# Performance work log

Measured on AMD Instinct MI355X. Metric: run time of the kernel, lower is better.

Reference implementation:

```python
import jax, jax.numpy as jnp
import numpy as np

D = 1024      # n_embedding
H = 16        # n_head
DH = D // H   # head_size = 64
T = 2048      # block_size / seq len
B = 2
EPS = 1e-5


def layer_norm(x, gamma, beta):
    mu = jnp.mean(x, axis=-1, keepdims=True)
    var = jnp.mean((x - mu) ** 2, axis=-1, keepdims=True)
    return (x - mu) * jax.lax.rsqrt(var + EPS) * gamma + beta


def setup_inputs() -> dict:
    key = jax.random.key(0)
    ks = jax.random.split(key, 12)
    s = 0.02
    return {
        "x": jax.random.normal(ks[0], (B, T, D), jnp.float32),
        # per-head QKV projections stacked over heads: [H, D, DH] (no bias, as in Head)
        "wq": jax.random.normal(ks[1], (H, D, DH), jnp.float32) * s,
        "wk": jax.random.normal(ks[2], (H, D, DH), jnp.float32) * s,
        "wv": jax.random.normal(ks[3], (H, D, DH), jnp.float32) * s,
        # output projection [H*DH, D] with bias
        "w_proj": jax.random.normal(ks[4], (H * DH, D), jnp.float32) * s,
        "b_proj": jnp.zeros((D,), jnp.float32),
        # feedforward: D -> 4D -> D
        "w1": jax.random.normal(ks[5], (D, 4 * D), jnp.float32) * s,
        "b1": jnp.zeros((4 * D,), jnp.float32),
        "w2": jax.random.normal(ks[6], (4 * D, D), jnp.float32) * s,
        "b2": jnp.zeros((D,), jnp.float32),
        # layer norms
        "ln1_g": jnp.ones((D,), jnp.float32),
        "ln1_b": jnp.zeros((D,), jnp.float32),
        "ln2_g": jnp.ones((D,), jnp.float32),
        "ln2_b": jnp.zeros((D,), jnp.float32),
    }


def reference(x, wq, wk, wv, w_proj, b_proj, w1, b1, w2, b2,
              ln1_g, ln1_b, ln2_g, ln2_b):
    # pre-LN attention sub-block
    xn = layer_norm(x, ln1_g, ln1_b)                      # [B,T,D]
    q = jnp.einsum('btd,hdk->bhtk', xn, wq)               # [B,H,T,DH]
    k = jnp.einsum('btd,hdk->bhtk', xn, wk)
    v = jnp.einsum('btd,hdk->bhtk', xn, wv)
    scale = DH ** -0.5
    scores = jnp.einsum('bhtk,bhsk->bhts', q, k) * scale  # [B,H,T,T]
    causal = jnp.tril(jnp.ones((T, T), bool))
    scores = jnp.where(causal, scores, -jnp.inf)
    attn = jax.nn.softmax(scores, axis=-1)
    out = jnp.einsum('bhts,bhsk->bhtk', attn, v)          # [B,H,T,DH]
    out = out.transpose(0, 2, 1, 3).reshape(B, T, H * DH)  # concat heads
    x = x + out @ w_proj + b_proj                          # residual 1
    # pre-LN feedforward sub-block
    xn2 = layer_norm(x, ln2_g, ln2_b)
    h = jax.nn.relu(xn2 @ w1 + b1)
    x = x + h @ w2 + b2                                    # residual 2
    return x
```

## Files before the change

### kernel.cpp

```cpp
#include <hip/hip_runtime.h>
#include <hip/hip_bf16.h>
#include <math.h>


#define D_MODEL 1024
#define NH 16
#define DHEAD 64
#define SEQ 2048
#define NTOK 4096

typedef __bf16 bf16x8 __attribute__((ext_vector_type(8)));
typedef float f32x4 __attribute__((ext_vector_type(4)));
typedef unsigned short u16x8 __attribute__((ext_vector_type(8)));

__device__ __forceinline__ unsigned short f2b(float f) {
  unsigned u = __builtin_bit_cast(unsigned, f);
  u = u + 0x7fffu + ((u >> 16) & 1u);
  return (unsigned short)(u >> 16);
}

__device__ __forceinline__ bf16x8 ld_bf16x8(const unsigned short* p) {
  u16x8 u = *(const u16x8*)p;
  return __builtin_bit_cast(bf16x8, u);
}

__device__ __forceinline__ void async16(void* lds, const void* g) {
  __builtin_amdgcn_global_load_lds(
      (const __attribute__((address_space(1))) unsigned int*)g,
      (__attribute__((address_space(3))) unsigned int*)lds, 16, 0, 0);
}


__global__ __launch_bounds__(256) void repack_qkv(
    const float* __restrict__ wq, const float* __restrict__ wk,
    const float* __restrict__ wv, unsigned short* __restrict__ outT) {
  __shared__ float tile[64][65];
  int t = blockIdx.x;
  int sel = t >> 8;
  int h = (t >> 4) & 15;
  int rt = t & 15;
  const float* in = (sel == 0 ? wq : sel == 1 ? wk : wv) + (size_t)h * D_MODEL * DHEAD;
  int d0 = rt * 64;
  for (int i = 0; i < 16; i++) {
    int idx = i * 256 + threadIdx.x;
    int r = idx >> 6, c = idx & 63;
    tile[r][c] = in[(size_t)(d0 + r) * DHEAD + c];
  }
  __syncthreads();
  unsigned short* ob = outT + (size_t)(sel * 1024 + h * 64) * D_MODEL + d0;
  for (int i = 0; i < 16; i++) {
    int idx = i * 256 + threadIdx.x;
    int c = idx >> 6, r = idx & 63;
    ob[(size_t)c * D_MODEL + r] = f2b(tile[r][c]);
  }
}

__global__ __launch_bounds__(256) void transpose_to_bf16(
    const float* __restrict__ in, unsigned short* __restrict__ out, int R, int C) {
  __shared__ float tile[64][65];
  int r0 = blockIdx.x * 64, c0 = blockIdx.y * 64;
  for (int i = 0; i < 16; i++) {
    int idx = i * 256 + threadIdx.x;
    int r = idx >> 6, c = idx & 63;
    tile[r][c] = in[(size_t)(r0 + r) * C + c0 + c];
  }
  __syncthreads();
  for (int i = 0; i < 16; i++) {
    int idx = i * 256 + threadIdx.x;
    int c = idx >> 6, r = idx & 63;
    out[(size_t)(c0 + c) * R + r0 + r] = f2b(tile[r][c]);
  }
}

__global__ __launch_bounds__(256) void layernorm_bf16(
    const float* __restrict__ x, const float* __restrict__ g,
    const float* __restrict__ bta, unsigned short* __restrict__ out) {
  int row = blockIdx.x;
  int tid = threadIdx.x;
  const float4* xr = (const float4*)(x + (size_t)row * D_MODEL);
  float4 v = xr[tid];
  float s = v.x + v.y + v.z + v.w;
  float s2 = v.x * v.x + v.y * v.y + v.z * v.z + v.w * v.w;
  for (int m = 1; m < 64; m <<= 1) {
    s += __shfl_xor(s, m);
    s2 += __shfl_xor(s2, m);
  }
  __shared__ float ps[4], ps2[4];
  int wid = tid >> 6;
  if ((tid & 63) == 0) { ps[wid] = s; ps2[wid] = s2; }
  __syncthreads();
  float S = ps[0] + ps[1] + ps[2] + ps[3];
  float S2 = ps2[0] + ps2[1] + ps2[2] + ps2[3];
  float mu = S * (1.f / D_MODEL);
  float var = S2 * (1.f / D_MODEL) - mu * mu;
  float inv = rsqrtf(var + 1e-5f);
  float4 gv = ((const float4*)g)[tid];
  float4 bv = ((const float4*)bta)[tid];
  ushort4 o;
  o.x = f2b((v.x - mu) * inv * gv.x + bv.x);
  o.y = f2b((v.y - mu) * inv * gv.y + bv.y);
  o.z = f2b((v.z - mu) * inv * gv.z + bv.z);
  o.w = f2b((v.w - mu) * inv * gv.w + bv.w);
  ((ushort4*)(out + (size_t)row * D_MODEL))[tid] = o;
}

template <int MODE>
__global__ __launch_bounds__(256, 2) void gemm_bt(
    const unsigned short* __restrict__ A, const unsigned short* __restrict__ BT,
    int M, int N, int K,
    const float* __restrict__ bias, const float* __restrict__ resid,
    float* __restrict__ outF, unsigned short* __restrict__ outB,
    unsigned short* __restrict__ outQ, unsigned short* __restrict__ outK,
    unsigned short* __restrict__ outV) {
  __shared__ alignas(16) unsigned short lsA[128 * 64];
  __shared__ alignas(16) unsigned short lsB[128 * 64];
  const int tid = threadIdx.x;
  const int wid = tid >> 6, lane = tid & 63;
  const int lr = lane & 15, lg = lane >> 4;
  const int row0 = blockIdx.x * 128, col0 = blockIdx.y * 128;
  const int wr = (wid >> 1) * 64, wc = (wid & 1) * 64;
  f32x4 acc[4][4] = {};
  const int nk = K >> 6;
  for (int kt = 0; kt < nk; ++kt) {
    const int k0 = kt << 6;
    if (kt) __syncthreads();
#pragma unroll
    for (int i = 0; i < 4; i++) {
      int sidx = i * 256 + tid;
      int r = sidx >> 3, s = sidx & 7;
      int ss = s ^ (r & 7);
      async16((char*)lsA + (i * 256 + wid * 64) * 16,
              A + (size_t)(row0 + r) * K + k0 + ss * 8);
      async16((char*)lsB + (i * 256 + wid * 64) * 16,
              BT + (size_t)(col0 + r) * K + k0 + ss * 8);
    }
    __syncthreads();
#pragma unroll
    for (int kk = 0; kk < 2; ++kk) {
      bf16x8 af[4], bfr[4];
#pragma unroll
      for (int m = 0; m < 4; m++) {
        int r = wr + m * 16 + lr;
        int sw = (kk * 4 + lg) ^ (r & 7);
        af[m] = *(const bf16x8*)((const char*)lsA + r * 128 + sw * 16);
      }
#pragma unroll
      for (int n = 0; n < 4; n++) {
        int r = wc + n * 16 + lr;
        int sw = (kk * 4 + lg) ^ (r & 7);
        bfr[n] = *(const bf16x8*)((const char*)lsB + r * 128 + sw * 16);
      }
#pragma unroll
      for (int m = 0; m < 4; m++)
#pragma unroll
        for (int n = 0; n < 4; n++)
          acc[m][n] = __builtin_amdgcn_mfma_f32_16x16x32_bf16(af[m], bfr[n], acc[m][n], 0, 0, 0);
    }
  }
#pragma unroll
  for (int m = 0; m < 4; m++) {
#pragma unroll
    for (int n = 0; n < 4; n++) {
#pragma unroll
      for (int r2 = 0; r2 < 4; r2++) {
        int row = row0 + wr + m * 16 + lg * 4 + r2;
        int col = col0 + wc + n * 16 + lr;
        float v = acc[m][n][r2];
        if constexpr (MODE == 0) {
          v += bias[col] + resid[(size_t)row * N + col];
          outF[(size_t)row * N + col] = v;
        } else if constexpr (MODE == 1) {
          v += bias[col];
          v = fmaxf(v, 0.f);
          outB[(size_t)row * N + col] = f2b(v);
        } else {
          int sel = col >> 10, jj = col & 1023, h = jj >> 6, dh = jj & 63;
          int b = row >> 11, t = row & 2047;
          size_t bh = (size_t)(b * NH + h);
          if (sel == 0)      outQ[(bh * SEQ + t) * DHEAD + dh] = f2b(v);
          else if (sel == 1) outK[(bh * SEQ + t) * DHEAD + dh] = f2b(v);
          else               outV[(bh * DHEAD + dh) * SEQ + t] = f2b(v);
        }
      }
    }
  }
}

__global__ __launch_bounds__(512, 2) void gemm_bt8(
    const unsigned short* __restrict__ A, const unsigned short* __restrict__ BT,
    int M, int N, int K,
    const float* __restrict__ bias, const float* __restrict__ resid,
    float* __restrict__ outF) {
  __shared__ alignas(16) unsigned short lsA[128 * 64];
  __shared__ alignas(16) unsigned short lsB[128 * 64];
  const int tid = threadIdx.x;
  const int wid = tid >> 6, lane = tid & 63;
  const int lr = lane & 15, lg = lane >> 4;
  const int row0 = blockIdx.x * 128, col0 = blockIdx.y * 128;
  const int wr = (wid >> 2) * 64, wc = (wid & 3) * 32;
  f32x4 acc[4][2] = {};
  const int nk = K >> 6;
  for (int kt = 0; kt < nk; ++kt) {
    const int k0 = kt << 6;
    if (kt) __syncthreads();
#pragma unroll
    for (int i = 0; i < 2; i++) {
      int sidx = i * 512 + tid;
      int r = sidx >> 3, s = sidx & 7;
      int ss = s ^ (r & 7);
      async16((char*)lsA + (i * 512 + wid * 64) * 16,
              A + (size_t)(row0 + r) * K + k0 + ss * 8);
      async16((char*)lsB + (i * 512 + wid * 64) * 16,
              BT + (size_t)(col0 + r) * K + k0 + ss * 8);
    }
    __syncthreads();
#pragma unroll
    for (int kk = 0; kk < 2; ++kk) {
      bf16x8 af[4], bfr[2];
#pragma unroll
      for (int m = 0; m < 4; m++) {
        int r = wr + m * 16 + lr;
        int sw = (kk * 4 + lg) ^ (r & 7);
        af[m] = *(const bf16x8*)((const char*)lsA + r * 128 + sw * 16);
      }
#pragma unroll
      for (int n = 0; n < 2; n++) {
        int r = wc + n * 16 + lr;
        int sw = (kk * 4 + lg) ^ (r & 7);
        bfr[n] = *(const bf16x8*)((const char*)lsB + r * 128 + sw * 16);
      }
#pragma unroll
      for (int m = 0; m < 4; m++)
#pragma unroll
        for (int n = 0; n < 2; n++)
          acc[m][n] = __builtin_amdgcn_mfma_f32_16x16x32_bf16(af[m], bfr[n], acc[m][n], 0, 0, 0);
    }
  }
#pragma unroll
  for (int m = 0; m < 4; m++) {
#pragma unroll
    for (int n = 0; n < 2; n++) {
#pragma unroll
      for (int r2 = 0; r2 < 4; r2++) {
        int row = row0 + wr + m * 16 + lg * 4 + r2;
        int col = col0 + wc + n * 16 + lr;
        float v = acc[m][n][r2] + bias[col] + resid[(size_t)row * N + col];
        outF[(size_t)row * N + col] = v;
      }
    }
  }
}

__global__ __launch_bounds__(512, 2) void gemm256_bt(
    const unsigned short* __restrict__ A, const unsigned short* __restrict__ BT,
    int M, int N, int K, int ntn,
    const float* __restrict__ bias, unsigned short* __restrict__ outB) {
  __shared__ alignas(16) unsigned short ls[2][2][2][256 * 32];
  const int tid = threadIdx.x;
  const int wid = tid >> 6, lane = tid & 63;
  const int lr = lane & 15, lg = lane >> 4;
  const int nwg = gridDim.x;
  const int wg = (blockIdx.x & 7) * (nwg >> 3) + (blockIdx.x >> 3);
  const int row0 = (wg / ntn) * 256, col0 = (wg % ntn) * 256;
  const int mbase = (wid >> 2) * 128;
  const int nbase = (wid & 3) * 64;

  f32x4 acc[8][4] = {};

  auto STAGE = [&](int buf, int kh, int ab, int kt) {
    const unsigned short* src = ab ? (BT + (size_t)col0 * K) : (A + (size_t)row0 * K);
    const int kbase = kt * 64 + kh * 32;
    unsigned short* dst0 = &ls[buf][kh][ab][0];
#pragma unroll
    for (int c = 0; c < 2; c++) {
      int s = c * 512 + tid;
      int row = s >> 2, c2 = s & 3;
      int ss = c2 ^ ((row >> 1) & 3);
      async16(dst0 + (size_t)(c * 512 + wid * 64) * 8,
              src + (size_t)row * K + kbase + ss * 8);
    }
  };
  auto LDA = [&](bf16x8* a, int buf, int kk, int mh) {
#pragma unroll
    for (int i = 0; i < 4; i++) {
      int mrow = mbase + (mh * 4 + i) * 16 + lr;
      int ch = lg ^ ((mrow >> 1) & 3);
      a[i] = *(const bf16x8*)&ls[buf][kk][0][mrow * 32 + ch * 8];
    }
  };
  auto LDB = [&](bf16x8* b, int buf, int kk) {
#pragma unroll
    for (int i = 0; i < 4; i++) {
      int brow = nbase + i * 16 + lr;
      int ch = lg ^ ((brow >> 1) & 3);
      b[i] = *(const bf16x8*)&ls[buf][kk][1][brow * 32 + ch * 8];
    }
  };

  const int nk = K >> 6;
  STAGE(0, 0, 0, 0); STAGE(0, 0, 1, 0); STAGE(0, 1, 0, 0); STAGE(0, 1, 1, 0);
  asm volatile("s_waitcnt vmcnt(4)" ::: "memory");
  __builtin_amdgcn_s_barrier();

  for (int t = 0; t < nk; ++t) {
    const int cur = t & 1, nxt = cur ^ 1;
    const bool haveNext = (t + 1 < nk);
    bf16x8 a[4], b[4];
    LDA(a, cur, 0, 0); LDB(b, cur, 0);
    if (haveNext) STAGE(nxt, 0, 0, t + 1);
    __builtin_amdgcn_s_barrier();
    asm volatile("s_waitcnt lgkmcnt(0)" ::: "memory");
    __builtin_amdgcn_sched_barrier(0);
    __builtin_amdgcn_s_setprio(1);
#pragma unroll
    for (int i = 0; i < 4; i++)
#pragma unroll
      for (int j = 0; j < 4; j++)
        acc[i][j] = __builtin_amdgcn_mfma_f32_16x16x32_bf16(a[i], b[j], acc[i][j], 0, 0, 0);
    __builtin_amdgcn_s_setprio(0);
    __builtin_amdgcn_s_barrier();
    LDA(a, cur, 0, 1);
    if (haveNext) {
      STAGE(nxt, 0, 1, t + 1);
      asm volatile("s_waitcnt vmcnt(4)" ::: "memory");
    } else {
      asm volatile("s_waitcnt vmcnt(0)" ::: "memory");
    }
    __builtin_amdgcn_s_barrier();
    asm volatile("s_waitcnt lgkmcnt(0)" ::: "memory");
    __builtin_amdgcn_sched_barrier(0);
    __builtin_amdgcn_s_setprio(1);
#pragma unroll
    for (int i = 0; i < 4; i++)
#pragma unroll
      for (int j = 0; j < 4; j++)
        acc[4 + i][j] = __builtin_amdgcn_mfma_f32_16x16x32_bf16(a[i], b[j], acc[4 + i][j], 0, 0, 0);
    __builtin_amdgcn_s_setprio(0);
    __builtin_amdgcn_s_barrier();
    LDA(a, cur, 1, 0); LDB(b, cur, 1);
    if (haveNext) STAGE(nxt, 1, 0, t + 1);
    __builtin_amdgcn_s_barrier();
    asm volatile("s_waitcnt lgkmcnt(0)" ::: "memory");
    __builtin_amdgcn_sched_barrier(0);
    __builtin_amdgcn_s_setprio(1);
#pragma unroll
    for (int i = 0; i < 4; i++)
#pragma unroll
      for (int j = 0; j < 4; j++)
        acc[i][j] = __builtin_amdgcn_mfma_f32_16x16x32_bf16(a[i], b[j], acc[i][j], 0, 0, 0);
    __builtin_amdgcn_s_setprio(0);
    __builtin_amdgcn_s_barrier();
    LDA(a, cur, 1, 1);
    if (haveNext) {
      STAGE(nxt, 1, 1, t + 1);
      asm volatile("s_waitcnt vmcnt(4)" ::: "memory");
    }
    __builtin_amdgcn_s_barrier();
    asm volatile("s_waitcnt lgkmcnt(0)" ::: "memory");
    __builtin_amdgcn_sched_barrier(0);
    __builtin_amdgcn_s_setprio(1);
#pragma unroll
    for (int i = 0; i < 4; i++)
#pragma unroll
      for (int j = 0; j < 4; j++)
        acc[4 + i][j] = __builtin_amdgcn_mfma_f32_16x16x32_bf16(a[i], b[j], acc[4 + i][j], 0, 0, 0);
    __builtin_amdgcn_s_setprio(0);
    __builtin_amdgcn_s_barrier();
  }
#pragma unroll
  for (int mi = 0; mi < 8; mi++) {
#pragma unroll
    for (int ni = 0; ni < 4; ni++) {
#pragma unroll
      for (int r2 = 0; r2 < 4; r2++) {
        int row = row0 + mbase + mi * 16 + lg * 4 + r2;
        int col = col0 + nbase + ni * 16 + lr;
        float v = acc[mi][ni][r2] + bias[col];
        outB[(size_t)row * N + col] = f2b(fmaxf(v, 0.f));
      }
    }
  }
}

__global__ __launch_bounds__(256) void attn_fwd(
    const unsigned short* __restrict__ Q, const unsigned short* __restrict__ K,
    const unsigned short* __restrict__ VT, unsigned short* __restrict__ O) {
  __shared__ alignas(16) unsigned short Kl[2][4096];
  __shared__ alignas(16) unsigned short Vl[2][4096];
  __shared__ alignas(16) unsigned short Plds[4][16][72];
  const int tid = threadIdx.x, wid = tid >> 6, lane = tid & 63;
  const int lr = lane & 15, lg = lane >> 4;
  const int sid = (int)(blockIdx.x & 7) * 128 + (int)(blockIdx.x >> 3);
  const int bh = sid >> 5, qt = 31 - (sid & 31);
  const unsigned short* Qb = Q + (size_t)bh * SEQ * DHEAD;
  const unsigned short* Kb = K + (size_t)bh * SEQ * DHEAD;
  const unsigned short* Vb = VT + (size_t)bh * DHEAD * SEQ;
  const int q0 = qt * 64 + wid * 16;
  bf16x8 qf[2];
#pragma unroll
  for (int kk = 0; kk < 2; kk++)
    qf[kk] = ld_bf16x8(Qb + (size_t)(q0 + lr) * DHEAD + kk * 32 + lg * 8);
  float psum[4] = {0.f, 0.f, 0.f, 0.f};
  f32x4 o[4] = {};
  const float cs = 0.18033688011112042f;
  const int ntiles = qt + 1;

  auto STAGE = [&](unsigned short* Kd, unsigned short* Vd, int s0) {
#pragma unroll
    for (int c = 0; c < 2; c++) {
      int s = c * 256 + tid;
      int row = s >> 3, sl = s & 7;
      int ss = sl ^ (row & 7);
      async16((char*)Kd + (c * 256 + wid * 64) * 16,
              Kb + (size_t)(s0 + row) * DHEAD + ss * 8);
      async16((char*)Vd + (c * 256 + wid * 64) * 16,
              Vb + (size_t)row * SEQ + s0 + ss * 8);
    }
  };

  STAGE(Kl[0], Vl[0], 0);
  for (int t = 0; t < ntiles; ++t) {
    if (t + 1 < ntiles) {
      STAGE(Kl[(t + 1) & 1], Vl[(t + 1) & 1], (t + 1) * 64);
      asm volatile("s_waitcnt vmcnt(4)" ::: "memory");
    } else {
      asm volatile("s_waitcnt vmcnt(0)" ::: "memory");
    }
    __builtin_amdgcn_s_barrier();
    __builtin_amdgcn_sched_barrier(0);
    const unsigned short* Kc = Kl[t & 1];
    const unsigned short* Vc = Vl[t & 1];
    const int s0 = t * 64;
    f32x4 sf[4];
#pragma unroll
    for (int n = 0; n < 4; n++) {
      f32x4 a = {};
#pragma unroll
      for (int kk = 0; kk < 2; kk++) {
        int r = n * 16 + lr;
        int ch = (kk * 4 + lg) ^ (r & 7);
        bf16x8 kf = *(const bf16x8*)((const char*)Kc + r * 128 + ch * 16);
        a = __builtin_amdgcn_mfma_f32_16x16x32_bf16(qf[kk], kf, a, 0, 0, 0);
      }
      sf[n] = a;
    }
    bf16x8 vfr[2][4];
#pragma unroll
    for (int kk2 = 0; kk2 < 2; kk2++)
#pragma unroll
      for (int j = 0; j < 4; j++) {
        int r = j * 16 + lr;
        int ch = (kk2 * 4 + lg) ^ (r & 7);
        vfr[kk2][j] = *(const bf16x8*)((const char*)Vc + r * 128 + ch * 16);
      }
    const bool needMask = (s0 + 63 > q0);
    float p[4][4];
#pragma unroll
    for (int n = 0; n < 4; n++)
#pragma unroll
      for (int r = 0; r < 4; r++) {
        float x = sf[n][r] * cs;
        if (needMask && (s0 + n * 16 + lr > q0 + lg * 4 + r)) x = -INFINITY;
        float e = __builtin_amdgcn_exp2f(x);
        p[n][r] = e;
        psum[r] += e;
      }
    asm volatile("" ::: "memory");
#pragma unroll
    for (int n = 0; n < 4; n++)
#pragma unroll
      for (int r = 0; r < 4; r++)
        Plds[wid][lg * 4 + r][n * 16 + lr] = f2b(p[n][r]);
    asm volatile("s_waitcnt lgkmcnt(0)" ::: "memory");
    __builtin_amdgcn_sched_barrier(0);
#pragma unroll
    for (int kk2 = 0; kk2 < 2; kk2++) {
      bf16x8 pa = *(const bf16x8*)&Plds[wid][lr][kk2 * 32 + lg * 8];
#pragma unroll
      for (int j = 0; j < 4; j++)
        o[j] = __builtin_amdgcn_mfma_f32_16x16x32_bf16(pa, vfr[kk2][j], o[j], 0, 0, 0);
    }
    __builtin_amdgcn_sched_barrier(0);
    __builtin_amdgcn_s_barrier();
  }
  unsigned short* Ob = O + ((size_t)(bh >> 4) * SEQ + q0) * D_MODEL + (bh & 15) * DHEAD;
#pragma unroll
  for (int r = 0; r < 4; r++) {
    float s = psum[r];
    s += __shfl_xor(s, 1);
    s += __shfl_xor(s, 2);
    s += __shfl_xor(s, 4);
    s += __shfl_xor(s, 8);
    float inv = 1.f / s;
#pragma unroll
    for (int j = 0; j < 4; j++)
      Ob[(size_t)(lg * 4 + r) * D_MODEL + j * 16 + lr] = f2b(o[j][r] * inv);
  }
}


extern "C" void kernel_launch(void* const* d_in, const int* in_sizes, int n_in,
                              void* d_out, int out_size, void* d_ws, size_t ws_size,
                              hipStream_t stream) {
  const float* x = (const float*)d_in[0];
  const float* wq = (const float*)d_in[1];
  const float* wk = (const float*)d_in[2];
  const float* wv = (const float*)d_in[3];
  const float* w_proj = (const float*)d_in[4];
  const float* b_proj = (const float*)d_in[5];
  const float* w1 = (const float*)d_in[6];
  const float* b1 = (const float*)d_in[7];
  const float* w2 = (const float*)d_in[8];
  const float* b2 = (const float*)d_in[9];
  const float* ln1g = (const float*)d_in[10];
  const float* ln1b = (const float*)d_in[11];
  const float* ln2g = (const float*)d_in[12];
  const float* ln2b = (const float*)d_in[13];

  char* ws = (char*)d_ws;
  const size_t MB = 1024ull * 1024ull;
  unsigned short* xn = (unsigned short*)(ws + 0);
  unsigned short* Qb = (unsigned short*)(ws + 8 * MB);
  unsigned short* Kb = (unsigned short*)(ws + 16 * MB);
  unsigned short* VTb = (unsigned short*)(ws + 24 * MB);
  unsigned short* aout = (unsigned short*)(ws + 32 * MB);
  unsigned short* hbuf = (unsigned short*)(ws + 40 * MB);
  unsigned short* WqkvT = (unsigned short*)(ws + 72 * MB);
  unsigned short* wprojT = (unsigned short*)(ws + 78 * MB);
  unsigned short* w1T = (unsigned short*)(ws + 80 * MB);
  unsigned short* w2T = (unsigned short*)(ws + 88 * MB);
  float* x1 = (float*)d_out;

  repack_qkv<<<dim3(768), 256, 0, stream>>>(wq, wk, wv, WqkvT);
  transpose_to_bf16<<<dim3(16, 16), 256, 0, stream>>>(w_proj, wprojT, 1024, 1024);
  transpose_to_bf16<<<dim3(16, 64), 256, 0, stream>>>(w1, w1T, 1024, 4096);
  transpose_to_bf16<<<dim3(64, 16), 256, 0, stream>>>(w2, w2T, 4096, 1024);

  layernorm_bf16<<<NTOK, 256, 0, stream>>>(x, ln1g, ln1b, xn);
  gemm_bt<2><<<dim3(32, 24), 256, 0, stream>>>(xn, WqkvT, NTOK, 3072, 1024,
      nullptr, nullptr, nullptr, nullptr, Qb, Kb, VTb);
  attn_fwd<<<dim3(1024), 256, 0, stream>>>(Qb, Kb, VTb, aout);
  gemm_bt8<<<dim3(32, 8), 512, 0, stream>>>(aout, wprojT, NTOK, 1024, 1024,
      b_proj, x, x1);
  layernorm_bf16<<<NTOK, 256, 0, stream>>>(x1, ln2g, ln2b, xn);
  gemm256_bt<<<dim3(256), 512, 0, stream>>>(xn, w1T, NTOK, 4096, 1024, 16,
      b1, hbuf);
  gemm_bt8<<<dim3(32, 8), 512, 0, stream>>>(hbuf, w2T, NTOK, 1024, 4096,
      b2, x1, (float*)d_out);
}
```

Baseline: 251.6 us.

## Triple-buffer LDS in gemm_bt8 with async prefetch two tiles ahead

Turns the single-buffered gemm_bt8 K-loop into a three-stage pipeline. Async global-to-LDS loads for tile kt+2 are issued while tile kt is computed, with explicit vmcnt waits and raw barriers. It also raises wave priority around the MFMA block and lowers launch bounds to one block per SM to fit 96KB of LDS. The goal is to hide global load latency, at the cost of occupancy.

```diff
diff --git a/kernel.cpp b/kernel.cpp
--- a/kernel.cpp
+++ b/kernel.cpp
@@ -186,13 +186,13 @@
   }
 }
 
-__global__ __launch_bounds__(512, 2) void gemm_bt8(
+__global__ __launch_bounds__(512, 1) void gemm_bt8(
     const unsigned short* __restrict__ A, const unsigned short* __restrict__ BT,
     int M, int N, int K,
     const float* __restrict__ bias, const float* __restrict__ resid,
     float* __restrict__ outF) {
-  __shared__ alignas(16) unsigned short lsA[128 * 64];
-  __shared__ alignas(16) unsigned short lsB[128 * 64];
+  __shared__ alignas(16) unsigned short lsA[3][128 * 64];
+  __shared__ alignas(16) unsigned short lsB[3][128 * 64];
   const int tid = threadIdx.x;
   const int wid = tid >> 6, lane = tid & 63;
   const int lr = lane & 15, lg = lane >> 4;
@@ -200,20 +200,35 @@
   const int wr = (wid >> 2) * 64, wc = (wid & 3) * 32;
   f32x4 acc[4][2] = {};
   const int nk = K >> 6;
-  for (int kt = 0; kt < nk; ++kt) {
+
+  auto STAGE = [&](int bi, int kt) {
     const int k0 = kt << 6;
-    if (kt) __syncthreads();
 #pragma unroll
     for (int i = 0; i < 2; i++) {
       int sidx = i * 512 + tid;
       int r = sidx >> 3, s = sidx & 7;
       int ss = s ^ (r & 7);
-      async16((char*)lsA + (i * 512 + wid * 64) * 16,
+      async16((char*)lsA[bi] + (i * 512 + wid * 64) * 16,
               A + (size_t)(row0 + r) * K + k0 + ss * 8);
-      async16((char*)lsB + (i * 512 + wid * 64) * 16,
+      async16((char*)lsB[bi] + (i * 512 + wid * 64) * 16,
               BT + (size_t)(col0 + r) * K + k0 + ss * 8);
     }
-    __syncthreads();
+  };
+
+  STAGE(0, 0);
+  if (nk > 1) STAGE(1, 1);
+  for (int kt = 0; kt < nk; ++kt) {
+    const int cur = kt % 3;
+    if (kt + 2 < nk) {
+      STAGE((kt + 2) % 3, kt + 2);
+      asm volatile("s_waitcnt vmcnt(8)" ::: "memory");
+    } else if (kt + 1 < nk) {
+      asm volatile("s_waitcnt vmcnt(4)" ::: "memory");
+    } else {
+      asm volatile("s_waitcnt vmcnt(0)" ::: "memory");
+    }
+    __builtin_amdgcn_s_barrier();
+    __builtin_amdgcn_sched_barrier(0);
 #pragma unroll
     for (int kk = 0; kk < 2; ++kk) {
       bf16x8 af[4], bfr[2];
@@ -221,20 +236,24 @@
       for (int m = 0; m < 4; m++) {
         int r = wr + m * 16 + lr;
         int sw = (kk * 4 + lg) ^ (r & 7);
-        af[m] = *(const bf16x8*)((const char*)lsA + r * 128 + sw * 16);
+        af[m] = *(const bf16x8*)((const char*)lsA[cur] + r * 128 + sw * 16);
       }
 #pragma unroll
       for (int n = 0; n < 2; n++) {
         int r = wc + n * 16 + lr;
         int sw = (kk * 4 + lg) ^ (r & 7);
-        bfr[n] = *(const bf16x8*)((const char*)lsB + r * 128 + sw * 16);
-      }
+        bfr[n] = *(const bf16x8*)((const char*)lsB[cur] + r * 128 + sw * 16);
+      }
+      __builtin_amdgcn_s_setprio(1);
 #pragma unroll
       for (int m = 0; m < 4; m++)
 #pragma unroll
         for (int n = 0; n < 2; n++)
           acc[m][n] = __builtin_amdgcn_mfma_f32_16x16x32_bf16(af[m], bfr[n], acc[m][n], 0, 0, 0);
-    }
+      __builtin_amdgcn_s_setprio(0);
+    }
+    __builtin_amdgcn_sched_barrier(0);
+    __builtin_amdgcn_s_barrier();
   }
 #pragma unroll
   for (int m = 0; m < 4; m++) {
```

Result: no change. 249.8 us (-0.7%).
